# Performance work log

Measured on AMD Instinct MI355X. Metric: run time of the kernel, lower is better.

Reference implementation:

```python
import jax, jax.numpy as jnp
import numpy as np

MAX_VAL = 255.0
C1 = (0.01 * MAX_VAL) ** 2
C2 = (0.03 * MAX_VAL) ** 2


def _gauss_window(ws, sigma, channel=3):
    x = np.arange(ws, dtype=np.float64)
    g = np.exp(-((x - ws // 2) ** 2) / (2.0 * sigma ** 2))
    g = g / g.sum()
    w2 = np.outer(g, g).astype(np.float32)  # [ws, ws]
    w = np.broadcast_to(w2, (channel, 1, ws, ws)).copy()  # depthwise OIHW
    return jnp.asarray(w)


def _dwconv(x, w, pad):
    # depthwise conv2d, NCHW, groups == channels
    return jax.lax.conv_general_dilated(
        x, w, window_strides=(1, 1), padding=[(pad, pad), (pad, pad)],
        dimension_numbers=("NCHW", "OIHW", "NCHW"),
        feature_group_count=x.shape[1])


def _ssim_pair(img1, img2):
    _, c, h, w = img1.shape
    ws = min(h, w, 11)
    sigma = 1.5 * ws / 11.0
    win = _gauss_window(ws, sigma, c)
    pad = ws // 2
    mu1 = _dwconv(img1, win, pad)
    mu2 = _dwconv(img2, win, pad)
    mu1_sq, mu2_sq, mu1_mu2 = mu1 * mu1, mu2 * mu2, mu1 * mu2
    sigma1_sq = _dwconv(img1 * img1, win, pad) - mu1_sq
    sigma2_sq = _dwconv(img2 * img2, win, pad) - mu2_sq
    sigma12 = _dwconv(img1 * img2, win, pad) - mu1_mu2
    V1 = 2.0 * sigma12 + C2
    V2 = sigma1_sq + sigma2_sq + C2
    ssim_map = (2.0 * mu1_mu2 + C1) * V1 / ((mu1_sq + mu2_sq + C1) * V2)
    mcs_map = V1 / V2
    return ssim_map.mean(), mcs_map.mean()


def _avg_pool2(x):
    B, C, H, W = x.shape
    return x.reshape(B, C, H // 2, 2, W // 2, 2).mean(axis=(3, 5))


def _ms_ssim(img1, img2, levels=5):
    weight = jnp.array([0.0448, 0.2856, 0.3001, 0.2363, 0.1333], jnp.float32)
    msssim, mcs = [], []
    for _ in range(levels):
        s, m = _ssim_pair(img1, img2)
        msssim.append(s)
        mcs.append(m)
        img1 = _avg_pool2(img1)
        img2 = _avg_pool2(img2)
    msssim = jnp.stack(msssim)
    mcs = jnp.stack(mcs)
    value = jnp.prod(mcs[: levels - 1] ** weight[: levels - 1]) * msssim[levels - 1] ** weight[levels - 1]
    return 1.0 - value


def _l1_oss(img1, img2):
    _, c, h, w = img1.shape
    ws = min(h, w, 7)
    sigma = 1.1 * ws / 7.0
    win = _gauss_window(ws, sigma, c)
    return _dwconv(jnp.abs(img1 - img2), win, ws // 2).mean()


def _clr_loss(img1, img3):
    _, c, h, w = img1.shape
    ws = min(h, w, 29)
    sigma = ws / 6.0
    win = _gauss_window(ws, sigma, c)
    pad = ws // 2
    mu1 = _dwconv(img1, win, pad)
    mu3 = _dwconv(img3, win, pad)
    cw = [-0.000519, 0.07633, -0.173433, 1.435936, -1.894404, 1.556091]
    # Horner evaluation of cw[5]*x^5 + ... + cw[1]*x + cw[0]
    mu1 = ((((cw[5] * mu1 + cw[4]) * mu1 + cw[3]) * mu1 + cw[2]) * mu1 + cw[1]) * mu1 + cw[0]
    wgray = jnp.array([0.299, 0.587, 0.144], jnp.float32).reshape(1, 3, 1, 1)
    mug1 = (mu1 * wgray).sum(axis=1, keepdims=True)  # 1x1 conv over channels
    mug3 = (mu3 * wgray).sum(axis=1, keepdims=True)
    me1 = mug1.mean(axis=(2, 3), keepdims=True)
    me3 = mug3.mean(axis=(2, 3), keepdims=True)
    sc = me1 / me3
    return jnp.abs(mu1 - mu3 * sc).mean()


def setup_inputs() -> dict:
    key = jax.random.key(0)
    k1, k2, k3 = jax.random.split(key, 3)
    shape = (16, 3, 512, 512)
    return {
        "img1": jax.random.uniform(k1, shape, dtype=jnp.float32),
        "img2": jax.random.uniform(k2, shape, dtype=jnp.float32),
        "img3": jax.random.uniform(k3, shape, dtype=jnp.float32),
    }


def reference(img1, img2, img3):
    l1v = _l1_oss(img1, img2)
    clrv = _clr_loss(img1, img3)
    ssimv = _ms_ssim(img1, img2)
    return 0.4 * ssimv + 0.4 * l1v + 0.2 * clrv
```

## Files before the change

kernel.cpp:

```cpp
#include <hip/hip_runtime.h>
#include <hip/hip_fp16.h>
#include <cmath>

typedef float f2 __attribute__((ext_vector_type(2)));

struct GW7  { float g[7];  };
struct GW11 { float g[11]; };
struct GW29 { float g[29]; };

static void make_gauss(int ws, double sigma, float* out) {
    double t[32]; double s = 0.0;
    int c = ws / 2;
    for (int i = 0; i < ws; ++i) { double d = i - c; t[i] = exp(-(d * d) / (2.0 * sigma * sigma)); s += t[i]; }
    for (int i = 0; i < ws; ++i) out[i] = (float)(t[i] / s);
}

#define ACC_SLOTS 44
#define ACC_BYTES (ACC_SLOTS * 64 * sizeof(double))

__device__ __forceinline__ float poly5(float x) {
    float r = fmaf(1.556091f, x, -1.894404f);
    r = fmaf(r, x, 1.435936f);
    r = fmaf(r, x, -0.173433f);
    r = fmaf(r, x, 0.07633f);
    r = fmaf(r, x, -0.000519f);
    return r;
}

__device__ __forceinline__ float border7(int p, const GW7& gw) {
    if (p >= 3 && p <= 508) return 1.f;
    float r = 0.f;
    #pragma unroll
    for (int k = 0; k < 7; ++k) { int q = p + 3 - k; if (q >= 0 && q < 512) r += gw.g[k]; }
    return r;
}

#define SSP 49
#define SRP 33
#define CLINE 33
#define CROWS 156

template<bool SRC2, bool INTERIOR>
__device__ __forceinline__ void ssim_tile(
    const float* __restrict__ Aim, const float* __restrict__ Bim,
    const f2* __restrict__ AB, int H, int plane, int ty, int tx,
    const GW11& gw, const GW7& g7, double* __restrict__ acc, int level,
    f2* __restrict__ pooled, int Ho, f2* lds, float* red, int bid)
{
    constexpr int IN = 42;
    f2* s    = lds;
    f2* r_mu = lds;
    f2* r_sq = lds + IN * SRP;

    const int tid = threadIdx.x;
    const size_t base = (size_t)plane * H * H;
    const int oy = ty * 32 - 5, ox = tx * 32 - 5;

    {
        int y = tid / 42;
        int x = tid - y * 42;
        #pragma unroll
        for (int it = 0; it < 7; ++it) {
            if (it < 6 || tid < 228) {
                f2 v;
                if (INTERIOR) {
                    size_t o = base + (size_t)(oy + y) * H + (ox + x);
                    if (SRC2) v = AB[o];
                    else { v.x = Aim[o]; v.y = Bim[o]; }
                } else {
                    int gy = oy + y, gx = ox + x;
                    bool ok = (gy >= 0) && (gy < H) && (gx >= 0) && (gx < H);
                    size_t o = base + (size_t)gy * H + gx;
                    v = (f2){0.f, 0.f};
                    if (ok) { if (SRC2) v = AB[o]; else { v.x = Aim[o]; v.y = Bim[o]; } }
                }
                s[y * SSP + x] = v;
            }
            y += 6; x += 4; if (x >= 42) { x -= 42; ++y; }
        }
    }
    __syncthreads();

    f2 v[18];
    const int ry = tid >> 2, rx0 = (tid & 3) * 8;
    if (tid < IN * 4) {
        #pragma unroll
        for (int l = 0; l < 18; ++l) v[l] = s[ry * SSP + rx0 + l];
    }
    if (pooled) {
        int py = tid >> 4, px = tid & 15;
        int a = (5 + 2 * py) * SSP + 5 + 2 * px;
        f2 u = s[a] + s[a + 1] + s[a + SSP] + s[a + SSP + 1];
        pooled[(size_t)plane * Ho * Ho + (size_t)(ty * 16 + py) * Ho + (tx * 16 + px)] = 0.25f * u;
    }
    float l1p = 0.f;
    if (level == 0) {
        #pragma unroll
        for (int jj = 0; jj < 4; ++jj) {
            int p = jj * 256 + tid;
            int py = p >> 5, px = p & 31;
            f2 u = s[(5 + py) * SSP + 5 + px];
            float d = fabsf(u.x - u.y);
            if (INTERIOR) l1p += d;
            else l1p += border7(ty * 32 + py, g7) * border7(tx * 32 + px, g7) * d;
        }
    }
    __syncthreads();

    if (tid < IN * 4) {
        #pragma unroll
        for (int j = 0; j < 8; ++j) {
            f2 a = {0.f, 0.f};
            #pragma unroll
            for (int k = 0; k < 11; ++k) a = gw.g[k] * v[j + k] + a;
            r_mu[ry * SRP + rx0 + j] = a;
        }
        #pragma unroll
        for (int l = 0; l < 18; ++l) {
            f2 w;
            w.x = fmaf(v[l].x, v[l].x, v[l].y * v[l].y);
            w.y = v[l].x * v[l].y;
            v[l] = w;
        }
        #pragma unroll
        for (int j = 0; j < 8; ++j) {
            f2 a = {0.f, 0.f};
            #pragma unroll
            for (int k = 0; k < 11; ++k) a = gw.g[k] * v[j + k] + a;
            r_sq[ry * SRP + rx0 + j] = a;
        }
    }
    __syncthreads();

    const int y0 = (tid >> 5) * 4, x = tid & 31;
    float lss = 0.f, lmc = 0.f;
    {
        f2 mu[4], q[4];
        {
            f2 u[14];
            #pragma unroll
            for (int l = 0; l < 14; ++l) u[l] = r_mu[(y0 + l) * SRP + x];
            #pragma unroll
            for (int j = 0; j < 4; ++j) {
                f2 a = {0.f, 0.f};
                #pragma unroll
                for (int k = 0; k < 11; ++k) a = gw.g[k] * u[j + k] + a;
                mu[j] = a;
            }
        }
        {
            f2 u[14];
            #pragma unroll
            for (int l = 0; l < 14; ++l) u[l] = r_sq[(y0 + l) * SRP + x];
            #pragma unroll
            for (int j = 0; j < 4; ++j) {
                f2 a = {0.f, 0.f};
                #pragma unroll
                for (int k = 0; k < 11; ++k) a = gw.g[k] * u[j + k] + a;
                q[j] = a;
            }
        }
        #pragma unroll
        for (int j = 0; j < 4; ++j) {
            float m1 = mu[j].x, m2 = mu[j].y;
            float P = m1 * m2;
            float S = fmaf(m1, m1, m2 * m2);
            float V1 = 2.f * (q[j].y - P) + 58.5225f;
            float V2 = (q[j].x - S) + 58.5225f;
            float num = (2.f * P + 6.5025f) * V1;
            float SC = S + 6.5025f;
            float inv = __builtin_amdgcn_rcpf(SC * V2);
            lss = fmaf(num, inv, lss);
            lmc = fmaf(V1 * SC, inv, lmc);
        }
    }
    #pragma unroll
    for (int o = 32; o > 0; o >>= 1) {
        lss += __shfl_down(lss, o); lmc += __shfl_down(lmc, o); l1p += __shfl_down(l1p, o);
    }
    if ((tid & 63) == 0) {
        int g = tid >> 6;
        red[g * 3] = lss; red[g * 3 + 1] = lmc; red[g * 3 + 2] = l1p;
    }
    __syncthreads();
    if (tid == 0) {
        float a = red[0] + red[3] + red[6] + red[9];
        float m = red[1] + red[4] + red[7] + red[10];
        int stripe = bid & 63;
        atomicAdd(&acc[(0 + level) * 64 + stripe], (double)a);
        atomicAdd(&acc[(5 + level) * 64 + stripe], (double)m);
        if (level == 0) {
            float l1 = red[2] + red[5] + red[8] + red[11];
            atomicAdd(&acc[10 * 64 + stripe], (double)l1);
        }
    }
}

template<bool SRC2>
__global__ __launch_bounds__(256, 8) void ssim_kernel(
    const float* __restrict__ Aim, const float* __restrict__ Bim, const f2* __restrict__ AB,
    int H, int tpp, int tilesX, GW11 gw, GW7 g7, double* __restrict__ acc, int level,
    f2* __restrict__ pooled, int Ho)
{
    __shared__ f2 lds[2 * 42 * SRP];
    __shared__ float red[12];
    const int bid = blockIdx.x;
    const int plane = bid / tpp;
    const int t = bid - plane * tpp;
    const int ty = t / tilesX, tx = t - ty * tilesX;
    const bool interior = (ty > 0) && (ty < tilesX - 1) && (tx > 0) && (tx < tilesX - 1);
    if (interior)
        ssim_tile<SRC2, true >(Aim, Bim, AB, H, plane, ty, tx, gw, g7, acc, level, pooled, Ho, lds, red, bid);
    else
        ssim_tile<SRC2, false>(Aim, Bim, AB, H, plane, ty, tx, gw, g7, acc, level, pooled, Ho, lds, red, bid);
}

template<bool CCLEAN>
__device__ __forceinline__ void clr_strip(
    const float* __restrict__ img1, const float* __restrict__ img3,
    int plane, int tx, int q, const GW29& gw, __half2* buf, float* red,
    double* __restrict__ acc, __half2* __restrict__ pbuf, int bid)
{
    const int tid = threadIdx.x;
    const int base_row = q * 128;
    const int b = plane / 3, c = plane - b * 3;
    const float wg = (c == 0) ? 0.299f : (c == 1 ? 0.587f : 0.144f);
    const size_t base = (size_t)plane * (512 * 512);
    const int rrow = tid >> 2, xq = tid & 3;
    const int c0 = tx * 8 + xq * 2 - 4;

    auto rowconv = [&](int rel) {
        __half2* dst = buf + (rel + 14) * CLINE + xq * 8;
        const int lr = base_row + rel;
        if (lr < 0 || lr >= 512) {
            #pragma unroll
            for (int j = 0; j < 8; ++j) dst[j] = __floats2half2_rn(0.f, 0.f);
            return;
        }
        const float4* row1 = (const float4*)(img1 + base + (size_t)lr * 512);
        const float4* row3 = (const float4*)(img3 + base + (size_t)lr * 512);
        float w[40];
        float o1[8];
        #pragma unroll
        for (int k = 0; k < 10; ++k) {
            float4 f;
            if (CCLEAN) f = row1[c0 + k];
            else {
                int cc = c0 + k;
                f = (float4){0.f, 0.f, 0.f, 0.f};
                if (cc >= 0 && cc < 128) f = row1[cc];
            }
            w[4 * k] = f.x; w[4 * k + 1] = f.y; w[4 * k + 2] = f.z; w[4 * k + 3] = f.w;
        }
        #pragma unroll
        for (int j = 0; j < 8; ++j) {
            float a = 0.f;
            #pragma unroll
            for (int k = 0; k < 29; ++k) a = fmaf(gw.g[k], w[2 + j + k], a);
            o1[j] = a;
        }
        #pragma unroll
        for (int k = 0; k < 10; ++k) {
            float4 f;
            if (CCLEAN) f = row3[c0 + k];
            else {
                int cc = c0 + k;
                f = (float4){0.f, 0.f, 0.f, 0.f};
                if (cc >= 0 && cc < 128) f = row3[cc];
            }
            w[4 * k] = f.x; w[4 * k + 1] = f.y; w[4 * k + 2] = f.z; w[4 * k + 3] = f.w;
        }
        #pragma unroll
        for (int j = 0; j < 8; ++j) {
            float a = 0.f;
            #pragma unroll
            for (int k = 0; k < 29; ++k) a = fmaf(gw.g[k], w[2 + j + k], a);
            dst[j] = __floats2half2_rn(o1[j], a);
        }
    };

    rowconv(-14 + rrow);
    __syncthreads();

    float p1 = 0.f, p3 = 0.f;
    const int x = tid & 31;
    #pragma unroll
    for (int ck = 0; ck < 2; ++ck) {
        int rel = 50 + 64 * ck + rrow;
        if (rel <= 141) rowconv(rel);
        __syncthreads();
        #pragma unroll
        for (int g = 0; g < 2; ++g) {
            const int y0 = 64 * ck + g * 32 + (tid >> 5) * 4;
            f2 u[32];
            #pragma unroll
            for (int l = 0; l < 32; ++l) {
                float2 tf = __half22float2(buf[(y0 + l) * CLINE + x]);
                u[l] = (f2){tf.x, tf.y};
            }
            #pragma unroll
            for (int j = 0; j < 4; ++j) {
                f2 a = {0.f, 0.f};
                #pragma unroll
                for (int k = 0; k < 29; ++k) a = gw.g[k] * u[j + k] + a;
                float p = poly5(a.x);
                p1 += p; p3 += a.y;
                pbuf[base + (size_t)(base_row + y0 + j) * 512 + (tx * 32 + x)] =
                    __floats2half2_rn(p, a.y);
            }
        }
    }

    p1 *= wg; p3 *= wg;
    #pragma unroll
    for (int o = 32; o > 0; o >>= 1) { p1 += __shfl_down(p1, o); p3 += __shfl_down(p3, o); }
    if ((tid & 63) == 0) { red[(tid >> 6) * 2] = p1; red[(tid >> 6) * 2 + 1] = p3; }
    __syncthreads();
    if (tid == 0) {
        float a1 = red[0] + red[2] + red[4] + red[6];
        float a3 = red[1] + red[3] + red[5] + red[7];
        int stripe = bid & 63;
        atomicAdd(&acc[(12 + b) * 64 + stripe], (double)a1);
        atomicAdd(&acc[(28 + b) * 64 + stripe], (double)a3);
    }
}

__global__ __launch_bounds__(256, 8) void fused_l0(
    const float* __restrict__ img1, const float* __restrict__ img2,
    const float* __restrict__ img3,
    GW11 g11, GW7 g7, GW29 g29,
    __half2* __restrict__ pbuf, f2* __restrict__ pooled, double* __restrict__ acc)
{
    __shared__ f2 lds[2 * 42 * SRP];
    __shared__ float red[12];
    const int bid = blockIdx.x;
    const int q5 = bid / 5;

    if (bid - q5 * 5 == 0) {
        const int cid = q5;
        __half2* buf = (__half2*)lds;
        const int plane = cid >> 6, rr = cid & 63;
        const int tx = rr >> 2, q = rr & 3;
        if (tx >= 1 && tx <= 14)
            clr_strip<true >(img1, img3, plane, tx, q, g29, buf, red, acc, pbuf, bid);
        else
            clr_strip<false>(img1, img3, plane, tx, q, g29, buf, red, acc, pbuf, bid);
        return;
    }

    const int sid = bid - q5 - 1;
    const int plane = sid >> 8;
    const int t = sid & 255;
    const int ty = t >> 4, tx = t & 15;
    const bool interior = (ty >= 1) && (ty <= 14) && (tx >= 1) && (tx <= 14);
    if (interior)
        ssim_tile<false, true >(img1, img2, nullptr, 512, plane, ty, tx, g11, g7, acc, 0, pooled, 256, lds, red, bid);
    else
        ssim_tile<false, false>(img1, img2, nullptr, 512, plane, ty, tx, g11, g7, acc, 0, pooled, 256, lds, red, bid);
}

#define CRP 33
#define RING 128
template<int MODE>
__global__ __launch_bounds__(256) void clr_conv(
    const float* __restrict__ img1, const float* __restrict__ img3,
    __half2* __restrict__ pbuf, GW29 gw, double* __restrict__ acc)
{
    __shared__ f2 r[RING * CRP];
    __shared__ float red[8];
    __shared__ float sc_sh;

    const int tid = threadIdx.x, bid = blockIdx.x;
    const int plane = bid >> 4, tx = bid & 15;
    const int b = plane / 3, c = plane - b * 3;
    const float wg = (c == 0) ? 0.299f : (c == 1 ? 0.587f : 0.144f);
    const size_t base = (size_t)plane * (512 * 512);

    if (MODE == 2 && tid < 64) {
        double m1 = acc[(12 + b) * 64 + tid];
        double m3 = acc[(28 + b) * 64 + tid];
        #pragma unroll
        for (int o = 32; o > 0; o >>= 1) { m1 += __shfl_down(m1, o); m3 += __shfl_down(m3, o); }
        if (tid == 0) sc_sh = (float)(m1 / m3);
    }

    const int rrow = tid >> 2, xq = tid & 3;
    const int c0 = tx * 8 + xq * 2 - 4;

    auto rowconv = [&](int lr) {
        const int ri = ((lr + RING) & (RING - 1)) * CRP + xq * 8;
        if (lr < 0 || lr >= 512) {
            #pragma unroll
            for (int j = 0; j < 8; ++j) r[ri + j] = (f2){0.f, 0.f};
            return;
        }
        const float4* row1 = (const float4*)(img1 + base + (size_t)lr * 512);
        const float4* row3 = (const float4*)(img3 + base + (size_t)lr * 512);
        float w[40];
        float o1[8];
        #pragma unroll
        for (int k = 0; k < 10; ++k) {
            int cc = c0 + k;
            float4 f = {0.f, 0.f, 0.f, 0.f};
            if (cc >= 0 && cc < 128) f = row1[cc];
            w[4 * k] = f.x; w[4 * k + 1] = f.y; w[4 * k + 2] = f.z; w[4 * k + 3] = f.w;
        }
        #pragma unroll
        for (int j = 0; j < 8; ++j) {
            float a = 0.f;
            #pragma unroll
            for (int k = 0; k < 29; ++k) a = fmaf(gw.g[k], w[2 + j + k], a);
            o1[j] = a;
        }
        #pragma unroll
        for (int k = 0; k < 10; ++k) {
            int cc = c0 + k;
            float4 f = {0.f, 0.f, 0.f, 0.f};
            if (cc >= 0 && cc < 128) f = row3[cc];
            w[4 * k] = f.x; w[4 * k + 1] = f.y; w[4 * k + 2] = f.z; w[4 * k + 3] = f.w;
        }
        #pragma unroll
        for (int j = 0; j < 8; ++j) {
            float a = 0.f;
            #pragma unroll
            for (int k = 0; k < 29; ++k) a = fmaf(gw.g[k], w[2 + j + k], a);
            r[ri + j] = (f2){o1[j], a};
        }
    };

    rowconv(-14 + rrow);
    __syncthreads();

    float p1 = 0.f, p3 = 0.f;
    const int x = tid & 31;
    #pragma unroll 1
    for (int ck = 0; ck < 8; ++ck) {
        {
            int lr = 50 + 64 * ck + rrow;
            if (lr <= 525) rowconv(lr);
        }
        __syncthreads();
        #pragma unroll
        for (int g = 0; g < 2; ++g) {
            const int y0 = 64 * ck + g * 32 + (tid >> 5) * 4;
            f2 u[32];
            #pragma unroll
            for (int l = 0; l < 32; ++l)
                u[l] = r[(((y0 - 14 + l) + RING) & (RING - 1)) * CRP + x];
            #pragma unroll
            for (int j = 0; j < 4; ++j) {
                f2 a = {0.f, 0.f};
                #pragma unroll
                for (int k = 0; k < 29; ++k) a = gw.g[k] * u[j + k] + a;
                float p = poly5(a.x);
                if (MODE == 2) {
                    p1 += fabsf(p - a.y * sc_sh);
                } else {
                    p1 += p; p3 += a.y;
                }
            }
        }
        if (ck < 7) __syncthreads();
    }

    if (MODE != 2) { p1 *= wg; p3 *= wg; }
    #pragma unroll
    for (int o = 32; o > 0; o >>= 1) { p1 += __shfl_down(p1, o); p3 += __shfl_down(p3, o); }
    if ((tid & 63) == 0) { red[(tid >> 6) * 2] = p1; red[(tid >> 6) * 2 + 1] = p3; }
    __syncthreads();
    if (tid == 0) {
        float a1 = red[0] + red[2] + red[4] + red[6];
        int stripe = bid & 63;
        if (MODE == 2) {
            atomicAdd(&acc[11 * 64 + stripe], (double)a1);
        } else {
            float a3 = red[1] + red[3] + red[5] + red[7];
            atomicAdd(&acc[(12 + b) * 64 + stripe], (double)a1);
            atomicAdd(&acc[(28 + b) * 64 + stripe], (double)a3);
        }
    }
}

__global__ __launch_bounds__(256) void clr_fin(
    const __half2* __restrict__ pbuf, double* __restrict__ acc)
{
    __shared__ float red[4];
    __shared__ float sc_sh;
    const int tid = threadIdx.x, bid = blockIdx.x;
    const int b = bid / 192, sub = bid - b * 192;
    if (tid < 64) {
        double m1 = acc[(12 + b) * 64 + tid];
        double m3 = acc[(28 + b) * 64 + tid];
        #pragma unroll
        for (int o = 32; o > 0; o >>= 1) { m1 += __shfl_down(m1, o); m3 += __shfl_down(m3, o); }
        if (tid == 0) sc_sh = (float)(m1 / m3);
    }
    __syncthreads();
    const float sc = sc_sh;
    const size_t bo = (size_t)b * 786432 + (size_t)sub * 4096;
    float s = 0.f;
    #pragma unroll
    for (int it = 0; it < 8; ++it) {
        size_t i = bo + it * 512 + tid * 2;
        float2 a = __half22float2(pbuf[i]);
        float2 c = __half22float2(pbuf[i + 1]);
        s += fabsf(a.x - a.y * sc) + fabsf(c.x - c.y * sc);
    }
    #pragma unroll
    for (int o = 32; o > 0; o >>= 1) s += __shfl_down(s, o);
    if ((tid & 63) == 0) red[tid >> 6] = s;
    __syncthreads();
    if (tid == 0)
        atomicAdd(&acc[11 * 64 + (bid & 63)], (double)(red[0] + red[1] + red[2] + red[3]));
}

__global__ void finalize_kernel(const double* __restrict__ acc, float* __restrict__ out)
{
    __shared__ double sums[ACC_SLOTS];
    int t = threadIdx.x;
    if (t < ACC_SLOTS) {
        double s = 0.0;
        for (int i = 0; i < 64; ++i) s += acc[t * 64 + i];
        sums[t] = s;
    }
    __syncthreads();
    if (t == 0) {
        const double w[5] = {0.0448, 0.2856, 0.3001, 0.2363, 0.1333};
        double value = 1.0;
        for (int l = 0; l < 5; ++l) {
            double dim = (double)(512 >> l);
            double cnt = 48.0 * dim * dim;
            double mval = (l < 4) ? (sums[5 + l] / cnt) : (sums[l] / cnt);
            value *= pow(mval, w[l]);
        }
        double n0 = 48.0 * 512.0 * 512.0;
        double l1v = sums[10] / n0;
        double clrv = sums[11] / n0;
        out[0] = (float)(0.4 * (1.0 - value) + 0.4 * l1v + 0.2 * clrv);
    }
}

extern "C" void kernel_launch(void* const* d_in, const int* in_sizes, int n_in,
                              void* d_out, int out_size, void* d_ws, size_t ws_size,
                              hipStream_t stream)
{
    (void)in_sizes; (void)n_in; (void)out_size;
    const float* img1 = (const float*)d_in[0];
    const float* img2 = (const float*)d_in[1];
    const float* img3 = (const float*)d_in[2];
    float* out = (float*)d_out;
    double* acc = (double*)d_ws;

    GW11 g11; make_gauss(11, 1.5, g11.g);
    GW7  g7;  make_gauss(7, 1.1, g7.g);
    GW29 g29; make_gauss(29, 29.0 / 6.0, g29.g);

    hipMemsetAsync(d_ws, 0, ACC_BYTES, stream);

    f2* pyr = (f2*)((char*)d_ws + 32768);
    size_t offs[4];
    offs[0] = 0;
    offs[1] = offs[0] + (size_t)48 * 256 * 256;
    offs[2] = offs[1] + (size_t)48 * 128 * 128;
    offs[3] = offs[2] + (size_t)48 * 64 * 64;
    const size_t PYRF2 = offs[3] + (size_t)48 * 32 * 32;

    const size_t poff = 32768 + PYRF2 * sizeof(f2);
    const size_t PBYTES = (size_t)48 * 512 * 512 * sizeof(__half2);
    __half2* pbuf = (__half2*)((char*)d_ws + poff);
    const bool bigws = (ws_size >= poff + PBYTES);

    if (bigws) {
        fused_l0<<<15360, 256, 0, stream>>>(img1, img2, img3, g11, g7, g29,
                                            pbuf, pyr + offs[0], acc);
    } else {
        ssim_kernel<false><<<12288, 256, 0, stream>>>(
            img1, img2, nullptr, 512, 256, 16, g11, g7, acc, 0, pyr + offs[0], 256);
        clr_conv<1><<<768, 256, 0, stream>>>(img1, img3, pbuf, g29, acc);
    }

    const f2* cur = pyr + offs[0];
    int H = 256;
    for (int l = 1; l < 5; ++l) {
        int tilesX = H / 32; int tpp = tilesX * tilesX;
        f2* pooled = (l < 4) ? (pyr + offs[l]) : nullptr;
        int Ho = H / 2;
        ssim_kernel<true><<<48 * tpp, 256, 0, stream>>>(
            nullptr, nullptr, cur, H, tpp, tilesX, g11, g7, acc, l, pooled, Ho);
        cur = pooled; H = Ho;
    }

    if (bigws) {
        clr_fin<<<3072, 256, 0, stream>>>(pbuf, acc);
    } else {
        clr_conv<2><<<768, 256, 0, stream>>>(img1, img3, pbuf, g29, acc);
    }

    finalize_kernel<<<1, 64, 0, stream>>>(acc, out);
}
```

Measured before the change: 217.4 us.

## Stream vertical convolutions, reuse one LDS buffer, use ring buffer in clr strip

Vertical Gaussian passes now accumulate four outputs while streaming rows from LDS, instead of first loading the whole column window into a register array. This cuts register pressure. The SSIM tile splits the mu and squared-moment passes into separate phases sharing a single LDS region, with extra barriers, so shared memory per block shrinks. The clr strip switches to a 128-row ring buffer in LDS. The launch-bounds occupancy hint is dropped, which gives the compiler more register freedom at the cost of the extra synchronization.

Result: faster. 208.6 us (-4.0%).

```diff
diff --git a/kernel.cpp b/kernel.cpp
--- a/kernel.cpp
+++ b/kernel.cpp
@@ -38,7 +38,6 @@
 #define SSP 49
 #define SRP 33
 #define CLINE 33
-#define CROWS 156
 
 template<bool SRC2, bool INTERIOR>
 __device__ __forceinline__ void ssim_tile(
@@ -48,9 +47,8 @@
     f2* __restrict__ pooled, int Ho, f2* lds, float* red, int bid)
 {
     constexpr int IN = 42;
-    f2* s    = lds;
-    f2* r_mu = lds;
-    f2* r_sq = lds + IN * SRP;
+    f2* s = lds;
+    f2* r = lds;
 
     const int tid = threadIdx.x;
     const size_t base = (size_t)plane * H * H;
@@ -113,8 +111,25 @@
             f2 a = {0.f, 0.f};
             #pragma unroll
             for (int k = 0; k < 11; ++k) a = gw.g[k] * v[j + k] + a;
-            r_mu[ry * SRP + rx0 + j] = a;
-        }
+            r[ry * SRP + rx0 + j] = a;
+        }
+    }
+    __syncthreads();
+
+    const int y0 = (tid >> 5) * 4, x = tid & 31;
+    f2 mu[4];
+    #pragma unroll
+    for (int j = 0; j < 4; ++j) mu[j] = (f2){0.f, 0.f};
+    #pragma unroll
+    for (int l = 0; l < 14; ++l) {
+        f2 val = r[(y0 + l) * SRP + x];
+        #pragma unroll
+        for (int j = 0; j < 4; ++j)
+            if (l - j >= 0 && l - j < 11) mu[j] = gw.g[l - j] * val + mu[j];
+    }
+    __syncthreads();
+
+    if (tid < IN * 4) {
         #pragma unroll
         for (int l = 0; l < 18; ++l) {
             f2 w;
@@ -127,38 +142,22 @@
             f2 a = {0.f, 0.f};
             #pragma unroll
             for (int k = 0; k < 11; ++k) a = gw.g[k] * v[j + k] + a;
-            r_sq[ry * SRP + rx0 + j] = a;
-        }
-    }
-    __syncthreads();
-
-    const int y0 = (tid >> 5) * 4, x = tid & 31;
+            r[ry * SRP + rx0 + j] = a;
+        }
+    }
+    __syncthreads();
+
     float lss = 0.f, lmc = 0.f;
     {
-        f2 mu[4], q[4];
-        {
-            f2 u[14];
-            #pragma unroll
-            for (int l = 0; l < 14; ++l) u[l] = r_mu[(y0 + l) * SRP + x];
-            #pragma unroll
-            for (int j = 0; j < 4; ++j) {
-                f2 a = {0.f, 0.f};
-                #pragma unroll
-                for (int k = 0; k < 11; ++k) a = gw.g[k] * u[j + k] + a;
-                mu[j] = a;
-            }
-        }
-        {
-            f2 u[14];
-            #pragma unroll
-            for (int l = 0; l < 14; ++l) u[l] = r_sq[(y0 + l) * SRP + x];
-            #pragma unroll
-            for (int j = 0; j < 4; ++j) {
-                f2 a = {0.f, 0.f};
-                #pragma unroll
-                for (int k = 0; k < 11; ++k) a = gw.g[k] * u[j + k] + a;
-                q[j] = a;
-            }
+        f2 q[4];
+        #pragma unroll
+        for (int j = 0; j < 4; ++j) q[j] = (f2){0.f, 0.f};
+        #pragma unroll
+        for (int l = 0; l < 14; ++l) {
+            f2 val = r[(y0 + l) * SRP + x];
+            #pragma unroll
+            for (int j = 0; j < 4; ++j)
+                if (l - j >= 0 && l - j < 11) q[j] = gw.g[l - j] * val + q[j];
         }
         #pragma unroll
         for (int j = 0; j < 4; ++j) {
@@ -197,12 +196,12 @@
 }
 
 template<bool SRC2>
-__global__ __launch_bounds__(256, 8) void ssim_kernel(
+__global__ __launch_bounds__(256) void ssim_kernel(
     const float* __restrict__ Aim, const float* __restrict__ Bim, const f2* __restrict__ AB,
     int H, int tpp, int tilesX, GW11 gw, GW7 g7, double* __restrict__ acc, int level,
     f2* __restrict__ pooled, int Ho)
 {
-    __shared__ f2 lds[2 * 42 * SRP];
+    __shared__ f2 lds[42 * SSP];
     __shared__ float red[12];
     const int bid = blockIdx.x;
     const int plane = bid / tpp;
@@ -230,7 +229,8 @@
     const int c0 = tx * 8 + xq * 2 - 4;
 
     auto rowconv = [&](int rel) {
-        __half2* dst = buf + (rel + 14) * CLINE + xq * 8;
+        const int slot = (rel + 128) & 127;
+        __half2* dst = buf + slot * CLINE + xq * 8;
         const int lr = base_row + rel;
         if (lr < 0 || lr >= 512) {
             #pragma unroll
@@ -292,23 +292,27 @@
         #pragma unroll
         for (int g = 0; g < 2; ++g) {
             const int y0 = 64 * ck + g * 32 + (tid >> 5) * 4;
-            f2 u[32];
+            f2 mu[4];
+            #pragma unroll
+            for (int j = 0; j < 4; ++j) mu[j] = (f2){0.f, 0.f};
             #pragma unroll
             for (int l = 0; l < 32; ++l) {
-                float2 tf = __half22float2(buf[(y0 + l) * CLINE + x]);
-                u[l] = (f2){tf.x, tf.y};
+                const int slot = (y0 - 14 + l + 128) & 127;
+                float2 tf = __half22float2(buf[slot * CLINE + x]);
+                f2 val = {tf.x, tf.y};
+                #pragma unroll
+                for (int j = 0; j < 4; ++j)
+                    if (l - j >= 0 && l - j < 29) mu[j] = gw.g[l - j] * val + mu[j];
             }
             #pragma unroll
             for (int j = 0; j < 4; ++j) {
-                f2 a = {0.f, 0.f};
-                #pragma unroll
-                for (int k = 0; k < 29; ++k) a = gw.g[k] * u[j + k] + a;
-                float p = poly5(a.x);
-                p1 += p; p3 += a.y;
+                float p = poly5(mu[j].x);
+                p1 += p; p3 += mu[j].y;
                 pbuf[base + (size_t)(base_row + y0 + j) * 512 + (tx * 32 + x)] =
-                    __floats2half2_rn(p, a.y);
+                    __floats2half2_rn(p, mu[j].y);
             }
         }
+        if (ck == 0) __syncthreads();
     }
 
     p1 *= wg; p3 *= wg;
@@ -325,13 +329,13 @@
     }
 }
 
-__global__ __launch_bounds__(256, 8) void fused_l0(
+__global__ __launch_bounds__(256) void fused_l0(
     const float* __restrict__ img1, const float* __restrict__ img2,
     const float* __restrict__ img3,
     GW11 g11, GW7 g7, GW29 g29,
     __half2* __restrict__ pbuf, f2* __restrict__ pooled, double* __restrict__ acc)
 {
-    __shared__ f2 lds[2 * 42 * SRP];
+    __shared__ f2 lds[2112];
     __shared__ float red[12];
     const int bid = blockIdx.x;
     const int q5 = bid / 5;
@@ -443,20 +447,23 @@
         #pragma unroll
         for (int g = 0; g < 2; ++g) {
             const int y0 = 64 * ck + g * 32 + (tid >> 5) * 4;
-            f2 u[32];
-            #pragma unroll
-            for (int l = 0; l < 32; ++l)
-                u[l] = r[(((y0 - 14 + l) + RING) & (RING - 1)) * CRP + x];
+            f2 mu[4];
+            #pragma unroll
+            for (int j = 0; j < 4; ++j) mu[j] = (f2){0.f, 0.f};
+            #pragma unroll
+            for (int l = 0; l < 32; ++l) {
+                f2 val = r[(((y0 - 14 + l) + RING) & (RING - 1)) * CRP + x];
+                #pragma unroll
+                for (int j = 0; j < 4; ++j)
+                    if (l - j >= 0 && l - j < 29) mu[j] = gw.g[l - j] * val + mu[j];
+            }
             #pragma unroll
             for (int j = 0; j < 4; ++j) {
-                f2 a = {0.f, 0.f};
-                #pragma unroll
-                for (int k = 0; k < 29; ++k) a = gw.g[k] * u[j + k] + a;
-                float p = poly5(a.x);
+                float p = poly5(mu[j].x);
                 if (MODE == 2) {
-                    p1 += fabsf(p - a.y * sc_sh);
+                    p1 += fabsf(p - mu[j].y * sc_sh);
                 } else {
-                    p1 += p; p3 += a.y;
+                    p1 += p; p3 += mu[j].y;
                 }
             }
         }
```
